# Performance work log

Measured on AMD Instinct MI355X. Metric: run time of the kernel, lower is better.

Reference implementation:

```python
import jax, jax.numpy as jnp
import numpy as np

B, T, D, H, L, W = 32, 512, 256, 8, 2, 10
NQ = 10000
HD = D // H


def setup_inputs():
    key = jax.random.key(0)
    ks = jax.random.split(key, 16)
    def n(k, shape, s=0.02):
        return jax.random.normal(k, shape, jnp.float32) * s
    return {
        "q": jax.random.randint(ks[0], (B, T), 0, NQ),
        "s": jax.random.randint(ks[1], (B, T), 0, 2),
        "q_embed": n(ks[2], (NQ + 1, D)),
        "s_embed": n(ks[3], (2, D)),
        "pos_embed": n(ks[4], (512, D)),
        "fusion_w": n(ks[5], (2 * D, D)),
        "fusion_b": jnp.zeros((D,), jnp.float32),
        "in_proj_w": n(ks[6], (L, D, 3 * D)),
        "in_proj_b": jnp.zeros((L, 3 * D), jnp.float32),
        "out_proj_w": n(ks[7], (L, D, D)),
        "out_proj_b": jnp.zeros((L, D), jnp.float32),
        "ln1_g": jnp.ones((L, D), jnp.float32),
        "ln1_b": jnp.zeros((L, D), jnp.float32),
        "ln2_g": jnp.ones((L, D), jnp.float32),
        "ln2_b": jnp.zeros((L, D), jnp.float32),
        "ff1_w": n(ks[8], (L, D, 4 * D)),
        "ff1_b": jnp.zeros((L, 4 * D), jnp.float32),
        "ff2_w": n(ks[9], (L, 4 * D, D)),
        "ff2_b": jnp.zeros((L, D), jnp.float32),
        "sw1": n(ks[10], (6, 32), 0.1),
        "sb1": jnp.zeros((32,), jnp.float32),
        "sw2": n(ks[11], (32, D // 4), 0.1),
        "sb2": jnp.zeros((D // 4,), jnp.float32),
        "cw1": n(ks[12], (D + D // 4, D)),
        "cb1": jnp.zeros((D,), jnp.float32),
        "cw2": n(ks[13], (D, 1)),
        "cb2": jnp.zeros((1,), jnp.float32),
    }


def _ln(x, g, b):
    mu = jnp.mean(x, -1, keepdims=True)
    var = jnp.mean(jnp.square(x - mu), -1, keepdims=True)
    return (x - mu) * jax.lax.rsqrt(var + 1e-5) * g + b


def _sliding_sum(x, w):
    # sum over trailing window of size w ending at each t, via prefix sums
    c = jnp.concatenate([jnp.zeros((x.shape[0], 1), x.dtype), jnp.cumsum(x, axis=1)], axis=1)
    t = jnp.arange(x.shape[1])
    return c[:, t + 1] - c[:, jnp.maximum(t + 1 - w, 0)]


def _stats(s, mask):
    # vectorized version of _extract_statistics (prefix-sum sliding windows)
    mf = mask.astype(jnp.float32)
    sf = s.astype(jnp.float32) * mf
    valid = _sliding_sum(mf, W)
    correct_rate = _sliding_sum(sf, W) / (valid + 1e-6)
    rc = _sliding_sum(mf, 5)
    recent_correct = _sliding_sum(sf, 5) / (rc + 1e-6)
    trans = ((s[:, 1:] != s[:, :-1]) & mask[:, 1:] & mask[:, :-1]).astype(jnp.float32)
    diff = jnp.concatenate([jnp.zeros((s.shape[0], 1), jnp.float32), trans], axis=1)
    change_rate = _sliding_sum(diff, W - 1) / (valid + 1e-6)
    # max consecutive equal run within each trailing window of size W
    sp = jnp.pad(s, ((0, 0), (W - 1, 0)))
    mp = jnp.pad(mask, ((0, 0), (W - 1, 0)))
    win_s = [sp[:, j:j + T] for j in range(W)]
    win_m = [mp[:, j:j + T] for j in range(W)]
    run = win_m[0].astype(jnp.float32)
    mx = run
    for j in range(1, W):  # fixed small window, not a data-dim loop
        eq = (win_s[j] == win_s[j - 1]) & win_m[j - 1]
        run = win_m[j].astype(jnp.float32) * (jnp.where(eq, run, 0.0) + 1.0)
        mx = jnp.maximum(mx, run)
    rel = jnp.broadcast_to(jnp.arange(T, dtype=jnp.float32) / max(T, 100), s.shape)
    cov = valid / W
    return jnp.stack([correct_rate, recent_correct, change_rate, mx / W, rel, cov], axis=-1)


def reference(q, s, q_embed, s_embed, pos_embed, fusion_w, fusion_b, in_proj_w, in_proj_b,
              out_proj_w, out_proj_b, ln1_g, ln1_b, ln2_g, ln2_b, ff1_w, ff1_b, ff2_w, ff2_b,
              sw1, sb1, sw2, sb2, cw1, cb1, cw2, cb2):
    mask = s >= 0
    qm = jnp.where(mask, q, 0)
    sm = jnp.where(mask, s, 0)
    h = jnp.concatenate([q_embed[qm], s_embed[sm]], axis=-1)  # [B,T,2D]
    h = jax.nn.relu(h @ fusion_w + fusion_b) + pos_embed[:T][None]
    causal = jnp.tril(jnp.ones((T, T), bool))
    allowed = causal[None, None] & mask[:, None, None, :]
    scale = 1.0 / (HD ** 0.5)
    for l in range(L):
        qkv = h @ in_proj_w[l] + in_proj_b[l]
        qh, kh, vh = jnp.split(qkv, 3, axis=-1)
        qh = qh.reshape(B, T, H, HD).transpose(0, 2, 1, 3)
        kh = kh.reshape(B, T, H, HD).transpose(0, 2, 1, 3)
        vh = vh.reshape(B, T, H, HD).transpose(0, 2, 1, 3)
        scores = jnp.einsum('bhqd,bhkd->bhqk', qh, kh) * scale
        scores = jnp.where(allowed, scores, -1e9)
        attn = jax.nn.softmax(scores, axis=-1)
        o = jnp.einsum('bhqk,bhkd->bhqd', attn, vh).transpose(0, 2, 1, 3).reshape(B, T, D)
        h = _ln(h + (o @ out_proj_w[l] + out_proj_b[l]), ln1_g[l], ln1_b[l])
        ff = jax.nn.gelu(h @ ff1_w[l] + ff1_b[l], approximate=False) @ ff2_w[l] + ff2_b[l]
        h = _ln(h + ff, ln2_g[l], ln2_b[l])
    sfeat = _stats(sm, mask)  # [B,T,6]
    semb = jax.nn.relu(sfeat @ sw1 + sb1) @ sw2 + sb2  # [B,T,D//4]
    comb = jnp.concatenate([h, semb], axis=-1)
    logits = (jax.nn.relu(comb @ cw1 + cb1) @ cw2 + cb2)[..., 0]
    return jnp.where(mask, logits, -1e9)
```

## Files before the change

kernel.cpp:

```cpp
#include <hip/hip_runtime.h>
#include <hip/hip_bf16.h>
#include <cmath>


using short8 = __attribute__((ext_vector_type(8))) short;
using short4v = __attribute__((ext_vector_type(4))) short;
using f32x4  = __attribute__((ext_vector_type(4))) float;

__device__ inline float gelu_f(float x) {
    return 0.5f * x * (1.0f + erff(x * 0.70710678118654752f));
}

__device__ inline short f2bf(float x) {
    union { float f; unsigned u; } v; v.f = x;
    return (short)((v.u + 0x7fffu + ((v.u >> 16) & 1u)) >> 16);
}

__device__ inline float bf2f(short v) {
    union { unsigned u; float f; } x; x.u = ((unsigned)(unsigned short)v) << 16;
    return x.f;
}

__device__ inline unsigned packbf(float lo, float hi) {
    union { float f; unsigned u; } a, b; a.f = lo; b.f = hi;
    unsigned ra = (a.u + 0x7fffu + ((a.u >> 16) & 1u)) >> 16;
    unsigned rb = (b.u + 0x7fffu + ((b.u >> 16) & 1u)) >> 16;
    return (rb << 16) | (ra & 0xffffu);
}

#define GLOAD16(gp, lp) __builtin_amdgcn_global_load_lds( \
    (const __attribute__((address_space(1))) void*)(gp), \
    (__attribute__((address_space(3))) void*)(lp), 16, 0, 0)

#define WAITVM(n) asm volatile("s_waitcnt vmcnt(" #n ")" ::: "memory")

__global__ __launch_bounds__(256) void prep_kernel(
    const float* __restrict__ fusion_w, const float* __restrict__ in_proj_w,
    const float* __restrict__ out_proj_w, const float* __restrict__ ff1_w,
    const float* __restrict__ ff2_w, const float* __restrict__ cw1,
    short* __restrict__ wts,
    const int* __restrict__ q, const int* __restrict__ s,
    const float* __restrict__ qe, const float* __restrict__ se,
    short* __restrict__ A)
{
    __shared__ float tile[32][33];
    if (blockIdx.x < 1744) {
        const int b0[10]      = {0,128,320,512,576,640,896,1152,1408,1664};
        const int Ks[10]      = {512,256,256,256,256,256,256,1024,1024,320};
        const int Ns[10]      = {256,768,768,256,256,1024,1024,256,256,256};
        const int sidx[10]    = {0,1,1,2,2,3,3,4,4,5};
        const size_t soff[10] = {0,0,196608,0,65536,0,262144,0,262144,0};
        const size_t doff[10] = {0,131072,327680,524288,589824,655360,917504,1179648,1441792,1703936};
        const float* srcs[6] = {fusion_w, in_proj_w, out_proj_w, ff1_w, ff2_w, cw1};
        int bid = blockIdx.x;
        int mi = 0;
        while (mi < 9 && bid >= b0[mi + 1]) ++mi;
        int bl = bid - b0[mi];
        int K = Ks[mi], N = Ns[mi];
        int tx = bl % (N >> 5), ty = bl / (N >> 5);
        const float* src = srcs[sidx[mi]] + soff[mi];
        short* dst = wts + doff[mi];
        int c = threadIdx.x & 31, r = threadIdx.x >> 5;
#pragma unroll
        for (int i = 0; i < 4; ++i)
            tile[r + i * 8][c] = src[(size_t)(ty * 32 + r + i * 8) * N + tx * 32 + c];
        __syncthreads();
#pragma unroll
        for (int i = 0; i < 4; ++i)
            dst[(size_t)(tx * 32 + r + i * 8) * K + ty * 32 + c] = f2bf(tile[c][r + i * 8]);
    } else {
        int e8 = (blockIdx.x - 1744) * 256 + threadIdx.x;
        int row = e8 >> 6;
        int k8 = (e8 & 63) << 3;
        int sv = s[row];
        bool mk = sv >= 0;
        const float* src = (k8 < 256) ? qe + (size_t)(mk ? q[row] : 0) * 256 + k8
                                      : se + (size_t)(mk ? sv : 0) * 256 + (k8 - 256);
        float4 v0 = *(const float4*)src;
        float4 v1 = *(const float4*)(src + 4);
        short8 o;
        o[0] = f2bf(v0.x); o[1] = f2bf(v0.y); o[2] = f2bf(v0.z); o[3] = f2bf(v0.w);
        o[4] = f2bf(v1.x); o[5] = f2bf(v1.y); o[6] = f2bf(v1.z); o[7] = f2bf(v1.w);
        *(short8*)(A + (size_t)row * 512 + k8) = o;
    }
}

template<int EPI, int BN, int K>
__global__ __launch_bounds__(512) void gemm_bstat(
    const short* __restrict__ A, const short* __restrict__ Wt,
    const float* __restrict__ bias, short* __restrict__ out0,
    short* __restrict__ ok, short* __restrict__ ov,
    const float* __restrict__ pos)
{
    constexpr int SPR = K / 8;
    constexpr int NSTEP = K / 32;
    constexpr int NJ = BN / 16;
    __shared__ short Bs[BN * K];
    const int tid = threadIdx.x, lane = tid & 63, wv = tid >> 6;
    const int lg = lane >> 4, lr = lane & 15;
    const int n0 = blockIdx.y * BN;
    const int row0 = blockIdx.x * 128 + wv * 16;

#pragma unroll
    for (int i = 0; i < (BN * K) / 4096; ++i) {
        int slot = i * 512 + tid;
        int n = slot / SPR, posn = slot % SPR;
        int g = posn ^ (n & 7);
        GLOAD16(Wt + (size_t)(n0 + n) * K + g * 8, &Bs[slot * 8]);
    }
    const short* arow = A + (size_t)(row0 + lr) * K;
    short8 af[NSTEP];
#pragma unroll
    for (int kk = 0; kk < NSTEP; ++kk)
        af[kk] = *(const short8*)(arow + kk * 32 + lg * 8);
    __syncthreads();

    f32x4 acc[NJ] = {};
#pragma unroll
    for (int kk = 0; kk < NSTEP; ++kk) {
#pragma unroll
        for (int j = 0; j < NJ; ++j) {
            int n = j * 16 + lr;
            short8 b = *(const short8*)&Bs[n * K + (((kk * 4 + lg) ^ (n & 7)) << 3)];
            acc[j] = __builtin_amdgcn_mfma_f32_16x16x32_bf16(af[kk], b, acc[j], 0, 0, 0);
        }
    }

    if constexpr (EPI == 0) {
#pragma unroll
        for (int j = 0; j < NJ; ++j)
#pragma unroll
        for (int r = 0; r < 4; ++r) {
            int row = row0 + lg * 4 + r;
            int col = n0 + j * 16 + lr;
            float x = acc[j][r] + bias[col];
            x = fmaxf(x, 0.f) + pos[(size_t)(row & 511) * 256 + col];
            out0[(size_t)row * 256 + col] = f2bf(x);
        }
    } else if constexpr (EPI == 1) {
#pragma unroll
        for (int j = 0; j < NJ; ++j)
#pragma unroll
        for (int r = 0; r < 4; ++r) {
            int row = row0 + lg * 4 + r;
            int gcol = n0 + j * 16 + lr;
            int t = row & 511, bg = row >> 9;
            int sec = gcol >> 8, cc = gcol & 255;
            int h = cc >> 5, d = cc & 31, bh = bg * 8 + h;
            short v = f2bf(acc[j][r] + bias[gcol]);
            if (sec == 0)      out0[((size_t)bh * 512 + t) * 32 + d] = v;
            else if (sec == 1) ok[((size_t)bh * 512 + t) * 32 + d] = v;
            else {
                int kl = t & 31;
                ov[(size_t)bh * 16384 + (size_t)(t >> 5) * 1024 +
                   (size_t)((kl >> 2) & 3) * 256 + d * 8 + (((kl & 3) << 1) | ((kl >> 4) & 1))] = v;
            }
        }
    } else {
#pragma unroll
        for (int j = 0; j < NJ; ++j)
#pragma unroll
        for (int r = 0; r < 4; ++r) {
            int row = row0 + lg * 4 + r;
            int gcol = n0 + j * 16 + lr;
            float x = acc[j][r] + bias[gcol];
            out0[(size_t)row * 1024 + gcol] = f2bf(gelu_f(x));
        }
    }
}

template<int EPI, int BM, int BN, int PANELS>
__global__ __launch_bounds__(256) void gemm_pipe(
    const short* __restrict__ A, const short* __restrict__ A2,
    const short* __restrict__ Wt, const float* __restrict__ bias,
    short* __restrict__ hb,
    const float* __restrict__ gamma, const float* __restrict__ beta,
    const float* __restrict__ cw2, const float* __restrict__ cb2,
    const int* __restrict__ smask, float* __restrict__ outlog, int N, int K)
{
    constexpr int WC = BN / 64;
    constexpr int L = BM / 64 + BN / 64;
    const int tid = threadIdx.x, lane = tid & 63, wv = tid >> 6;
    const int lg = lane >> 4, lr = lane & 15;
    const int wr = wv / WC, wc = wv % WC;
    const int bid = blockIdx.x;
    const int p = (bid >> 3) % PANELS;
    const int y = ((bid >> 3) / PANELS) * 8 + (bid & 7);
    const int m0 = y * BM, n0 = p * BN;

    __shared__ short As[3][BM * 32];
    __shared__ short Bs[3][BN * 32];
    __shared__ float redS[64][4];
    __shared__ float redQ[64][4];

    f32x4 acc[4][4] = {};
    const int nsteps = K >> 5;

    auto stage = [&](int buf, int step) {
        int k0 = step << 5;
#pragma unroll
        for (int i = 0; i < BM / 64; ++i) {
            int slot = i * 256 + tid;
            int g = slot / BM, m = slot % BM;
            int k = k0 + g * 8;
            const short* src;
            if constexpr (EPI == 4)
                src = (k < 256) ? A + (size_t)(m0 + m) * 256 + k
                                : A2 + (size_t)(m0 + m) * 64 + (k - 256);
            else
                src = A + (size_t)(m0 + m) * K + k;
            GLOAD16(src, &As[buf][slot * 8]);
        }
#pragma unroll
        for (int i = 0; i < BN / 64; ++i) {
            int slot = i * 256 + tid;
            int g = slot / BN, n = slot % BN;
            GLOAD16(Wt + (size_t)(n0 + n) * K + k0 + g * 8, &Bs[buf][slot * 8]);
        }
    };

    stage(0, 0);
    stage(1, 1);
    int cur = 0;
    for (int t = 0; t < nsteps; ++t) {
        if (t + 2 < nsteps) {
            int c2 = cur + 2; if (c2 >= 3) c2 -= 3;
            stage(c2, t + 2);
            if constexpr (L == 4) WAITVM(8); else WAITVM(10);
        } else if (t + 1 < nsteps) {
            if constexpr (L == 4) WAITVM(4); else WAITVM(5);
        } else {
            WAITVM(0);
        }
        __builtin_amdgcn_s_barrier();
        __builtin_amdgcn_sched_barrier(0);
        short8 a[4], b[4];
#pragma unroll
        for (int i = 0; i < 4; ++i)
            a[i] = *(const short8*)&As[cur][(lg * BM + wr * 64 + i * 16 + lr) * 8];
#pragma unroll
        for (int j = 0; j < 4; ++j)
            b[j] = *(const short8*)&Bs[cur][(lg * BN + wc * 64 + j * 16 + lr) * 8];
#pragma unroll
        for (int i = 0; i < 4; ++i)
#pragma unroll
            for (int j = 0; j < 4; ++j)
                acc[i][j] = __builtin_amdgcn_mfma_f32_16x16x32_bf16(a[i], b[j], acc[i][j], 0, 0, 0);
        __builtin_amdgcn_sched_barrier(0);
        __builtin_amdgcn_s_barrier();
        cur = (cur == 2) ? 0 : cur + 1;
    }

    if constexpr (EPI == 3) {
        float ps[4][4], pq[4][4];
#pragma unroll
        for (int i = 0; i < 4; ++i)
#pragma unroll
        for (int r = 0; r < 4; ++r) { ps[i][r] = 0.f; pq[i][r] = 0.f; }
#pragma unroll
        for (int i = 0; i < 4; ++i)
#pragma unroll
        for (int j = 0; j < 4; ++j)
#pragma unroll
        for (int r = 0; r < 4; ++r) {
            int row = m0 + i * 16 + lg * 4 + r;
            int col = wc * 64 + j * 16 + lr;
            float x = acc[i][j][r] + bias[col] + bf2f(hb[(size_t)row * 256 + col]);
            acc[i][j][r] = x;
            ps[i][r] += x; pq[i][r] += x * x;
        }
#pragma unroll
        for (int off = 1; off < 16; off <<= 1)
#pragma unroll
            for (int i = 0; i < 4; ++i)
#pragma unroll
            for (int r = 0; r < 4; ++r) {
                ps[i][r] += __shfl_xor(ps[i][r], off);
                pq[i][r] += __shfl_xor(pq[i][r], off);
            }
        if (lr == 0) {
#pragma unroll
            for (int i = 0; i < 4; ++i)
#pragma unroll
            for (int r = 0; r < 4; ++r) {
                int rl = i * 16 + lg * 4 + r;
                redS[rl][wc] = ps[i][r]; redQ[rl][wc] = pq[i][r];
            }
        }
        __syncthreads();
#pragma unroll
        for (int i = 0; i < 4; ++i)
#pragma unroll
        for (int r = 0; r < 4; ++r) {
            int rl = i * 16 + lg * 4 + r;
            int row = m0 + rl;
            float sm = redS[rl][0] + redS[rl][1] + redS[rl][2] + redS[rl][3];
            float sq = redQ[rl][0] + redQ[rl][1] + redQ[rl][2] + redQ[rl][3];
            float mu = sm * (1.f / 256.f);
            float var = sq * (1.f / 256.f) - mu * mu;
            float rstd = rsqrtf(var + 1e-5f);
#pragma unroll
            for (int j = 0; j < 4; ++j) {
                int col = wc * 64 + j * 16 + lr;
                float yv = (acc[i][j][r] - mu) * rstd * gamma[col] + beta[col];
                hb[(size_t)row * 256 + col] = f2bf(yv);
            }
        }
    } else {
        float pa[4][4];
#pragma unroll
        for (int i = 0; i < 4; ++i)
#pragma unroll
        for (int r = 0; r < 4; ++r) pa[i][r] = 0.f;
#pragma unroll
        for (int i = 0; i < 4; ++i)
#pragma unroll
        for (int j = 0; j < 4; ++j)
#pragma unroll
        for (int r = 0; r < 4; ++r) {
            int col = wc * 64 + j * 16 + lr;
            float x = fmaxf(acc[i][j][r] + bias[col], 0.f);
            pa[i][r] += x * cw2[col];
        }
#pragma unroll
        for (int off = 1; off < 16; off <<= 1)
#pragma unroll
            for (int i = 0; i < 4; ++i)
#pragma unroll
            for (int r = 0; r < 4; ++r) pa[i][r] += __shfl_xor(pa[i][r], off);
        if (lr == 0) {
#pragma unroll
            for (int i = 0; i < 4; ++i)
#pragma unroll
            for (int r = 0; r < 4; ++r)
                redS[i * 16 + lg * 4 + r][wc] = pa[i][r];
        }
        __syncthreads();
        if (tid < 64) {
            int row = m0 + tid;
            float v = redS[tid][0] + redS[tid][1] + redS[tid][2] + redS[tid][3] + cb2[0];
            outlog[row] = (smask[row] >= 0) ? v : -1e9f;
        }
    }
}

__global__ __launch_bounds__(256) void attn_mfma(
    const short* __restrict__ Qg, const short* __restrict__ Kg,
    const short* __restrict__ VTg, short* __restrict__ O)
{
    __shared__ unsigned Wp[4][16][20];
    const int bh = blockIdx.x >> 2, part = blockIdx.x & 3;
    const int b = bh >> 3, h = bh & 7;
    const int wv = threadIdx.x >> 6, lane = threadIdx.x & 63;
    const int lg = lane >> 4, lr = lane & 15;
    const int slot = part * 4 + wv;
    const short* Qbh = Qg + (size_t)bh * 16384;
    const short* Kbh = Kg + (size_t)bh * 16384;
    const short* Vbh = VTg + (size_t)bh * 16384;
    const float scale = 0.17677669529663687f;

    for (int half = 0; half < 2; ++half) {
        const int tile = half ? (31 - slot) : slot;
        const int q0 = tile << 4;
        short8 qa = *(const short8*)(Qbh + (size_t)(q0 + lr) * 32 + lg * 8);
        f32x4 o0 = {}, o1 = {};
        float l_[4] = {0.f, 0.f, 0.f, 0.f};
        const int nfull = q0 >> 5;

        for (int c = 0; c <= nfull; ++c) {
            int kc = c << 5;
            short8 kf0 = *(const short8*)(Kbh + (size_t)(kc + lr) * 32 + lg * 8);
            short8 kf1 = *(const short8*)(Kbh + (size_t)(kc + 16 + lr) * 32 + lg * 8);
            f32x4 s0 = {}, s1 = {};
            s0 = __builtin_amdgcn_mfma_f32_16x16x32_bf16(qa, kf0, s0, 0, 0, 0);
            s1 = __builtin_amdgcn_mfma_f32_16x16x32_bf16(qa, kf1, s1, 0, 0, 0);
            float p0[4], p1[4];
            if (c < nfull) {
#pragma unroll
                for (int r = 0; r < 4; ++r) {
                    p0[r] = __expf(s0[r] * scale);
                    p1[r] = __expf(s1[r] * scale);
                }
            } else {
#pragma unroll
                for (int r = 0; r < 4; ++r) {
                    int qq = q0 + lg * 4 + r;
                    p0[r] = (kc + lr)      > qq ? 0.f : __expf(s0[r] * scale);
                    p1[r] = (kc + 16 + lr) > qq ? 0.f : __expf(s1[r] * scale);
                }
            }
#pragma unroll
            for (int r = 0; r < 4; ++r) {
                l_[r] += p0[r] + p1[r];
                Wp[wv][lg * 4 + r][lr] = packbf(p0[r], p1[r]);
            }
            short8 pa = *(const short8*)&Wp[wv][lr][lg * 4];
            short8 vf0 = *(const short8*)(Vbh + (size_t)c * 1024 + lg * 256 + lr * 8);
            short8 vf1 = *(const short8*)(Vbh + (size_t)c * 1024 + lg * 256 + (lr + 16) * 8);
            o0 = __builtin_amdgcn_mfma_f32_16x16x32_bf16(pa, vf0, o0, 0, 0, 0);
            o1 = __builtin_amdgcn_mfma_f32_16x16x32_bf16(pa, vf1, o1, 0, 0, 0);
        }
#pragma unroll
        for (int off = 1; off < 16; off <<= 1)
#pragma unroll
            for (int r = 0; r < 4; ++r) l_[r] += __shfl_xor(l_[r], off);
#pragma unroll
        for (int r = 0; r < 4; ++r) {
            float inv = 1.f / l_[r];
            size_t ro = ((size_t)b * 512 + q0 + lg * 4 + r) * 256 + h * 32;
            O[ro + lr] = f2bf(o0[r] * inv);
            O[ro + 16 + lr] = f2bf(o1[r] * inv);
        }
    }
}

__global__ __launch_bounds__(512) void stats_kernel(
    const int* __restrict__ s, short* __restrict__ semb,
    const float* __restrict__ sw1, const float* __restrict__ sb1,
    const float* __restrict__ sw2, const float* __restrict__ sb2)
{
    __shared__ float sv_sh[512];
    __shared__ float m_sh[512];
    __shared__ float sw2_sh[2048];
    const int b = blockIdx.x;
    const int t = threadIdx.x;
    {
        int sval = s[b * 512 + t];
        bool mk = sval >= 0;
        sv_sh[t] = mk ? (float)sval : 0.f;
        m_sh[t] = mk ? 1.f : 0.f;
    }
    for (int i = t; i < 2048; i += 512) sw2_sh[i] = sw2[i];
    __syncthreads();

    float mf10 = 0, sf10 = 0, mf5 = 0, sf5 = 0, d9 = 0;
#pragma unroll
    for (int k = 0; k < 10; ++k) {
        int idx = t - k;
        if (idx >= 0) {
            float mv = m_sh[idx], sv = sv_sh[idx];
            mf10 += mv; sf10 += sv;
            if (k < 5) { mf5 += mv; sf5 += sv; }
            if (k < 9 && idx >= 1) {
                if (sv != sv_sh[idx - 1] && mv > 0.5f && m_sh[idx - 1] > 0.5f) d9 += 1.f;
            }
        }
    }
    float run, mx;
    {
        int x0 = t - 9;
        run = (x0 >= 0) ? m_sh[x0] : 0.f;
        mx = run;
#pragma unroll
        for (int j = 1; j < 10; ++j) {
            int xc = t + j - 9, xp = xc - 1;
            float sc = (xc >= 0) ? sv_sh[xc] : 0.f;
            float sp = (xp >= 0) ? sv_sh[xp] : 0.f;
            float mc = (xc >= 0) ? m_sh[xc] : 0.f;
            float mp = (xp >= 0) ? m_sh[xp] : 0.f;
            bool eq = (sc == sp) && (mp > 0.5f);
            run = (mc > 0.5f) ? ((eq ? run : 0.f) + 1.f) : 0.f;
            mx = fmaxf(mx, run);
        }
    }
    float f[6];
    f[0] = sf10 / (mf10 + 1e-6f);
    f[1] = sf5 / (mf5 + 1e-6f);
    f[2] = d9 / (mf10 + 1e-6f);
    f[3] = mx * 0.1f;
    f[4] = (float)t * (1.f / 512.f);
    f[5] = mf10 * 0.1f;

    float hid[32];
#pragma unroll
    for (int j2 = 0; j2 < 32; ++j2) {
        float a = sb1[j2];
#pragma unroll
        for (int i = 0; i < 6; ++i) a = fmaf(f[i], sw1[i * 32 + j2], a);
        hid[j2] = fmaxf(a, 0.f);
    }
    short* orow = semb + ((size_t)b * 512 + t) * 64;
    for (int c = 0; c < 64; c += 4) {
        float v0 = sb2[c], v1 = sb2[c + 1], v2 = sb2[c + 2], v3 = sb2[c + 3];
#pragma unroll
        for (int j2 = 0; j2 < 32; ++j2) {
            float hh = hid[j2];
            v0 = fmaf(hh, sw2_sh[j2 * 64 + c], v0);
            v1 = fmaf(hh, sw2_sh[j2 * 64 + c + 1], v1);
            v2 = fmaf(hh, sw2_sh[j2 * 64 + c + 2], v2);
            v3 = fmaf(hh, sw2_sh[j2 * 64 + c + 3], v3);
        }
        short4v o; o[0] = f2bf(v0); o[1] = f2bf(v1); o[2] = f2bf(v2); o[3] = f2bf(v3);
        *(short4v*)(orow + c) = o;
    }
}

extern "C" void kernel_launch(void* const* d_in, const int* in_sizes, int n_in,
                              void* d_out, int out_size, void* d_ws, size_t ws_size,
                              hipStream_t stream) {
    const int*   q         = (const int*)d_in[0];
    const int*   s         = (const int*)d_in[1];
    const float* q_embed   = (const float*)d_in[2];
    const float* s_embed   = (const float*)d_in[3];
    const float* pos_embed = (const float*)d_in[4];
    const float* fusion_w  = (const float*)d_in[5];
    const float* fusion_b  = (const float*)d_in[6];
    const float* in_proj_w = (const float*)d_in[7];
    const float* in_proj_b = (const float*)d_in[8];
    const float* out_proj_w= (const float*)d_in[9];
    const float* out_proj_b= (const float*)d_in[10];
    const float* ln1_g     = (const float*)d_in[11];
    const float* ln1_b     = (const float*)d_in[12];
    const float* ln2_g     = (const float*)d_in[13];
    const float* ln2_b     = (const float*)d_in[14];
    const float* ff1_w     = (const float*)d_in[15];
    const float* ff1_b     = (const float*)d_in[16];
    const float* ff2_w     = (const float*)d_in[17];
    const float* ff2_b     = (const float*)d_in[18];
    const float* sw1       = (const float*)d_in[19];
    const float* sb1       = (const float*)d_in[20];
    const float* sw2       = (const float*)d_in[21];
    const float* sb2       = (const float*)d_in[22];
    const float* cw1       = (const float*)d_in[23];
    const float* cb1       = (const float*)d_in[24];
    const float* cw2       = (const float*)d_in[25];
    const float* cb2       = (const float*)d_in[26];
    float* out = (float*)d_out;

    char* base = (char*)d_ws;
    short* hb   = (short*)(base);
    short* bufA = (short*)(base + 8388608);
    short* att  = (short*)(base + 41943040);
    short* Qg   = (short*)(base + 50331648);
    short* Kg   = (short*)(base + 58720256);
    short* VTg  = (short*)(base + 67108864);
    short* semb = (short*)(base + 75497472);
    short* wts  = (short*)(base + 77594624);

    const size_t W_FUSION = 0, W_INPROJ0 = 131072, W_INPROJ1 = 327680;
    const size_t W_OUTPROJ0 = 524288, W_OUTPROJ1 = 589824;
    const size_t W_FF1_0 = 655360, W_FF1_1 = 917504;
    const size_t W_FF2_0 = 1179648, W_FF2_1 = 1441792;
    const size_t W_CW1 = 1703936;

    prep_kernel<<<5840, 256, 0, stream>>>(fusion_w, in_proj_w, out_proj_w,
                                          ff1_w, ff2_w, cw1, wts,
                                          q, s, q_embed, s_embed, bufA);
    gemm_bstat<0, 64, 512><<<dim3(128, 4), 512, 0, stream>>>(bufA,
        wts + W_FUSION, fusion_b, hb, nullptr, nullptr, pos_embed);
    for (int l = 0; l < 2; ++l) {
        gemm_bstat<1, 128, 256><<<dim3(128, 6), 512, 0, stream>>>(hb,
            wts + (l ? W_INPROJ1 : W_INPROJ0), in_proj_b + l * 768,
            Qg, Kg, VTg, nullptr);
        attn_mfma<<<1024, 256, 0, stream>>>(Qg, Kg, VTg, att);
        gemm_pipe<3, 64, 256, 1><<<256, 256, 0, stream>>>(att, nullptr,
            wts + (l ? W_OUTPROJ1 : W_OUTPROJ0), out_proj_b + l * 256,
            hb, ln1_g + l * 256, ln1_b + l * 256,
            nullptr, nullptr, nullptr, nullptr, 256, 256);
        gemm_bstat<2, 128, 256><<<dim3(128, 8), 512, 0, stream>>>(hb,
            wts + (l ? W_FF1_1 : W_FF1_0), ff1_b + l * 1024,
            bufA, nullptr, nullptr, nullptr);
        gemm_pipe<3, 64, 256, 1><<<256, 256, 0, stream>>>(bufA, nullptr,
            wts + (l ? W_FF2_1 : W_FF2_0), ff2_b + l * 256,
            hb, ln2_g + l * 256, ln2_b + l * 256,
            nullptr, nullptr, nullptr, nullptr, 256, 1024);
    }
    stats_kernel<<<32, 512, 0, stream>>>(s, semb, sw1, sb1, sw2, sb2);
    gemm_pipe<4, 64, 256, 1><<<256, 256, 0, stream>>>(hb, semb,
        wts + W_CW1, cb1, nullptr, nullptr, nullptr,
        cw2, cb2, s, out, 256, 320);
}
```

Before: 303.7 us.

## Replace triple-buffered 256-thread row GEMM with 512-thread double-buffered variant

The full-row GEMMs with fused residual+LayerNorm and classifier epilogues now use 512 threads (8 waves, 2x4 layout) per 64x256 tile. Each wave holds half as many accumulators, and the pipeline goes from triple buffering with explicit vmcnt waits to double buffering with __syncthreads. More waves per block should hide latency better and ease register pressure. The cost is a shallower prefetch and a full barrier every K step.

```diff
diff --git a/kernel.cpp b/kernel.cpp
--- a/kernel.cpp
+++ b/kernel.cpp
@@ -31,8 +31,6 @@
 #define GLOAD16(gp, lp) __builtin_amdgcn_global_load_lds( \
     (const __attribute__((address_space(1))) void*)(gp), \
     (__attribute__((address_space(3))) void*)(lp), 16, 0, 0)
-
-#define WAITVM(n) asm volatile("s_waitcnt vmcnt(" #n ")" ::: "memory")
 
 __global__ __launch_bounds__(256) void prep_kernel(
     const float* __restrict__ fusion_w, const float* __restrict__ in_proj_w,
@@ -169,101 +167,84 @@
     }
 }
 
-template<int EPI, int BM, int BN, int PANELS>
-__global__ __launch_bounds__(256) void gemm_pipe(
+template<int EPI>
+__global__ __launch_bounds__(512) void gemm_red(
     const short* __restrict__ A, const short* __restrict__ A2,
     const short* __restrict__ Wt, const float* __restrict__ bias,
     short* __restrict__ hb,
     const float* __restrict__ gamma, const float* __restrict__ beta,
     const float* __restrict__ cw2, const float* __restrict__ cb2,
-    const int* __restrict__ smask, float* __restrict__ outlog, int N, int K)
+    const int* __restrict__ smask, float* __restrict__ outlog, int K)
 {
-    constexpr int WC = BN / 64;
-    constexpr int L = BM / 64 + BN / 64;
     const int tid = threadIdx.x, lane = tid & 63, wv = tid >> 6;
     const int lg = lane >> 4, lr = lane & 15;
-    const int wr = wv / WC, wc = wv % WC;
-    const int bid = blockIdx.x;
-    const int p = (bid >> 3) % PANELS;
-    const int y = ((bid >> 3) / PANELS) * 8 + (bid & 7);
-    const int m0 = y * BM, n0 = p * BN;
-
-    __shared__ short As[3][BM * 32];
-    __shared__ short Bs[3][BN * 32];
+    const int wr = wv >> 2, wc = wv & 3;
+    const int m0 = blockIdx.x * 64;
+
+    __shared__ short As[2][2048];
+    __shared__ short Bs[2][8192];
     __shared__ float redS[64][4];
     __shared__ float redQ[64][4];
 
-    f32x4 acc[4][4] = {};
+    f32x4 acc[2][4] = {};
     const int nsteps = K >> 5;
 
     auto stage = [&](int buf, int step) {
         int k0 = step << 5;
-#pragma unroll
-        for (int i = 0; i < BM / 64; ++i) {
-            int slot = i * 256 + tid;
-            int g = slot / BM, m = slot % BM;
-            int k = k0 + g * 8;
-            const short* src;
+        if (tid < 256) {
+            int k = k0 + wv * 8;
+            const short* srcA;
             if constexpr (EPI == 4)
-                src = (k < 256) ? A + (size_t)(m0 + m) * 256 + k
-                                : A2 + (size_t)(m0 + m) * 64 + (k - 256);
+                srcA = (k < 256) ? A + (size_t)(m0 + lane) * 256 + k
+                                 : A2 + (size_t)(m0 + lane) * 64 + (k - 256);
             else
-                src = A + (size_t)(m0 + m) * K + k;
-            GLOAD16(src, &As[buf][slot * 8]);
-        }
-#pragma unroll
-        for (int i = 0; i < BN / 64; ++i) {
-            int slot = i * 256 + tid;
-            int g = slot / BN, n = slot % BN;
-            GLOAD16(Wt + (size_t)(n0 + n) * K + k0 + g * 8, &Bs[buf][slot * 8]);
+                srcA = A + (size_t)(m0 + lane) * K + k;
+            GLOAD16(srcA, &As[buf][(wv * 64) * 8]);
+        }
+        {
+            GLOAD16(Wt + (size_t)(tid & 255) * K + k0 + (tid >> 8) * 8,
+                    &Bs[buf][(wv * 64) * 8]);
+        }
+        {
+            int slot = tid + 512;
+            GLOAD16(Wt + (size_t)(slot & 255) * K + k0 + (slot >> 8) * 8,
+                    &Bs[buf][((wv + 8) * 64) * 8]);
         }
     };
 
     stage(0, 0);
-    stage(1, 1);
-    int cur = 0;
-    for (int t = 0; t < nsteps; ++t) {
-        if (t + 2 < nsteps) {
-            int c2 = cur + 2; if (c2 >= 3) c2 -= 3;
-            stage(c2, t + 2);
-            if constexpr (L == 4) WAITVM(8); else WAITVM(10);
-        } else if (t + 1 < nsteps) {
-            if constexpr (L == 4) WAITVM(4); else WAITVM(5);
-        } else {
-            WAITVM(0);
-        }
-        __builtin_amdgcn_s_barrier();
-        __builtin_amdgcn_sched_barrier(0);
-        short8 a[4], b[4];
-#pragma unroll
-        for (int i = 0; i < 4; ++i)
-            a[i] = *(const short8*)&As[cur][(lg * BM + wr * 64 + i * 16 + lr) * 8];
+    __syncthreads();
+    for (int step = 0; step < nsteps; ++step) {
+        int cur = step & 1;
+        if (step + 1 < nsteps) stage(cur ^ 1, step + 1);
+        short8 a[2], b[4];
+#pragma unroll
+        for (int i = 0; i < 2; ++i)
+            a[i] = *(const short8*)&As[cur][(lg * 64 + wr * 32 + i * 16 + lr) * 8];
 #pragma unroll
         for (int j = 0; j < 4; ++j)
-            b[j] = *(const short8*)&Bs[cur][(lg * BN + wc * 64 + j * 16 + lr) * 8];
-#pragma unroll
-        for (int i = 0; i < 4; ++i)
+            b[j] = *(const short8*)&Bs[cur][(lg * 256 + wc * 64 + j * 16 + lr) * 8];
+#pragma unroll
+        for (int i = 0; i < 2; ++i)
 #pragma unroll
             for (int j = 0; j < 4; ++j)
                 acc[i][j] = __builtin_amdgcn_mfma_f32_16x16x32_bf16(a[i], b[j], acc[i][j], 0, 0, 0);
-        __builtin_amdgcn_sched_barrier(0);
-        __builtin_amdgcn_s_barrier();
-        cur = (cur == 2) ? 0 : cur + 1;
+        __syncthreads();
     }
 
     if constexpr (EPI == 3) {
-        float ps[4][4], pq[4][4];
-#pragma unroll
-        for (int i = 0; i < 4; ++i)
+        float ps[2][4], pq[2][4];
+#pragma unroll
+        for (int i = 0; i < 2; ++i)
 #pragma unroll
         for (int r = 0; r < 4; ++r) { ps[i][r] = 0.f; pq[i][r] = 0.f; }
 #pragma unroll
-        for (int i = 0; i < 4; ++i)
+        for (int i = 0; i < 2; ++i)
 #pragma unroll
         for (int j = 0; j < 4; ++j)
 #pragma unroll
         for (int r = 0; r < 4; ++r) {
-            int row = m0 + i * 16 + lg * 4 + r;
+            int row = m0 + wr * 32 + i * 16 + lg * 4 + r;
             int col = wc * 64 + j * 16 + lr;
             float x = acc[i][j][r] + bias[col] + bf2f(hb[(size_t)row * 256 + col]);
             acc[i][j][r] = x;
@@ -272,7 +253,7 @@
 #pragma unroll
         for (int off = 1; off < 16; off <<= 1)
 #pragma unroll
-            for (int i = 0; i < 4; ++i)
+            for (int i = 0; i < 2; ++i)
 #pragma unroll
             for (int r = 0; r < 4; ++r) {
                 ps[i][r] += __shfl_xor(ps[i][r], off);
@@ -280,19 +261,19 @@
             }
         if (lr == 0) {
 #pragma unroll
-            for (int i = 0; i < 4; ++i)
+            for (int i = 0; i < 2; ++i)
 #pragma unroll
             for (int r = 0; r < 4; ++r) {
-                int rl = i * 16 + lg * 4 + r;
+                int rl = wr * 32 + i * 16 + lg * 4 + r;
                 redS[rl][wc] = ps[i][r]; redQ[rl][wc] = pq[i][r];
             }
         }
         __syncthreads();
 #pragma unroll
-        for (int i = 0; i < 4; ++i)
-#pragma unroll
-        for (int r = 0; r < 4; ++r) {
-            int rl = i * 16 + lg * 4 + r;
+        for (int i = 0; i < 2; ++i)
+#pragma unroll
+        for (int r = 0; r < 4; ++r) {
+            int rl = wr * 32 + i * 16 + lg * 4 + r;
             int row = m0 + rl;
             float sm = redS[rl][0] + redS[rl][1] + redS[rl][2] + redS[rl][3];
             float sq = redQ[rl][0] + redQ[rl][1] + redQ[rl][2] + redQ[rl][3];
@@ -307,13 +288,13 @@
             }
         }
     } else {
-        float pa[4][4];
-#pragma unroll
-        for (int i = 0; i < 4; ++i)
+        float pa[2][4];
+#pragma unroll
+        for (int i = 0; i < 2; ++i)
 #pragma unroll
         for (int r = 0; r < 4; ++r) pa[i][r] = 0.f;
 #pragma unroll
-        for (int i = 0; i < 4; ++i)
+        for (int i = 0; i < 2; ++i)
 #pragma unroll
         for (int j = 0; j < 4; ++j)
 #pragma unroll
@@ -325,15 +306,15 @@
 #pragma unroll
         for (int off = 1; off < 16; off <<= 1)
 #pragma unroll
-            for (int i = 0; i < 4; ++i)
+            for (int i = 0; i < 2; ++i)
 #pragma unroll
             for (int r = 0; r < 4; ++r) pa[i][r] += __shfl_xor(pa[i][r], off);
         if (lr == 0) {
 #pragma unroll
-            for (int i = 0; i < 4; ++i)
+            for (int i = 0; i < 2; ++i)
 #pragma unroll
             for (int r = 0; r < 4; ++r)
-                redS[i * 16 + lg * 4 + r][wc] = pa[i][r];
+                redS[wr * 32 + i * 16 + lg * 4 + r][wc] = pa[i][r];
         }
         __syncthreads();
         if (tid < 64) {
@@ -553,20 +534,20 @@
             wts + (l ? W_INPROJ1 : W_INPROJ0), in_proj_b + l * 768,
             Qg, Kg, VTg, nullptr);
         attn_mfma<<<1024, 256, 0, stream>>>(Qg, Kg, VTg, att);
-        gemm_pipe<3, 64, 256, 1><<<256, 256, 0, stream>>>(att, nullptr,
+        gemm_red<3><<<256, 512, 0, stream>>>(att, nullptr,
             wts + (l ? W_OUTPROJ1 : W_OUTPROJ0), out_proj_b + l * 256,
             hb, ln1_g + l * 256, ln1_b + l * 256,
-            nullptr, nullptr, nullptr, nullptr, 256, 256);
+            nullptr, nullptr, nullptr, nullptr, 256);
         gemm_bstat<2, 128, 256><<<dim3(128, 8), 512, 0, stream>>>(hb,
             wts + (l ? W_FF1_1 : W_FF1_0), ff1_b + l * 1024,
             bufA, nullptr, nullptr, nullptr);
-        gemm_pipe<3, 64, 256, 1><<<256, 256, 0, stream>>>(bufA, nullptr,
+        gemm_red<3><<<256, 512, 0, stream>>>(bufA, nullptr,
             wts + (l ? W_FF2_1 : W_FF2_0), ff2_b + l * 256,
             hb, ln2_g + l * 256, ln2_b + l * 256,
-            nullptr, nullptr, nullptr, nullptr, 256, 1024);
+            nullptr, nullptr, nullptr, nullptr, 1024);
     }
     stats_kernel<<<32, 512, 0, stream>>>(s, semb, sw1, sb1, sw2, sb2);
-    gemm_pipe<4, 64, 256, 1><<<256, 256, 0, stream>>>(hb, semb,
+    gemm_red<4><<<256, 512, 0, stream>>>(hb, semb,
         wts + W_CW1, cb1, nullptr, nullptr, nullptr,
-        cw2, cb2, s, out, 256, 320);
-}
+        cw2, cb2, s, out, 320);
+}
```

Result: faster. 281.4 us (-7.3%).
